# Optimization experiments

Hardware: AMD Instinct MI355X
Metric: run time of the kernel (lower is better)

Reference implementation:

```python
import jax, jax.numpy as jnp
import numpy as np

SIZE = 14          # feature-map side (448 image / stride 32)
IMG_STRIDE = 32    # feature->image coordinate stride
RATIOS = [(4, 4), (3, 5), (5, 3), (6, 6), (5, 7), (7, 5), (8, 8), (6, 10), (10, 6)]
GROUPS = [(0, 3), (3, 6), (6, 9)]   # ratio index ranges per scale group
N_LIST = [3, 2, 1]                   # proposals kept per group (sum = proposalN = 6)
IOU_THRESHS = [0.25, 0.25, 0.25]
WIN_NUMS = [(SIZE - h + 1) * (SIZE - w + 1) for h, w in RATIOS]  # 121,120,120,81,80,80,49,45,45
OFFS = np.cumsum([0] + WIN_NUMS)


def _make_coords():
    # image-space [x0,y0,x1,y1] per window, same order as flattened avgpool outputs
    coords = []
    for h, w in RATIOS:
        Ho, Wo = SIZE - h + 1, SIZE - w + 1
        for i in range(Ho):
            for j in range(Wo):
                x0 = i * IMG_STRIDE - 1
                y0 = j * IMG_STRIDE - 1
                x1 = x0 + h * IMG_STRIDE
                y1 = y0 + w * IMG_STRIDE
                coords.append([max(x0, 0), max(y0, 0), x1, y1])
    return np.asarray(coords, np.int32)  # [741, 4]


def setup_inputs() -> dict:
    key = jax.random.key(0)
    B = 65536
    x = jax.random.normal(key, (B, 1, SIZE, SIZE), dtype=jnp.float32)
    coords = jnp.asarray(_make_coords())
    return {"x": x, "coords": coords, "proposalN": 6}


def _avgpool_scores(x):
    # x: [B,1,H,W] -> concat of flattened VALID avgpools, [B, sum(WIN_NUMS)]
    B = x.shape[0]
    outs = []
    for h, w in RATIOS:
        s = jax.lax.reduce_window(x, 0.0, jax.lax.add, (1, 1, h, w), (1, 1, 1, 1), 'VALID')
        outs.append((s / (h * w)).reshape(B, -1))
    return jnp.concatenate(outs, axis=1)


def _nms_group(scores, coords_f, areas, N, thresh):
    # greedy NMS: repeatedly take argmax of remaining scores, suppress IoU>thresh.
    # Matches the torch/numpy loop (sorted-walk == repeated argmax for distinct scores).
    W = scores.shape[0]
    def step(carry, _):
        mask, last = carry
        any_v = jnp.any(mask)
        idx = jnp.argmax(jnp.where(mask, scores, -jnp.inf)).astype(jnp.int32)
        idx = jnp.where(any_v, idx, last)  # if exhausted, repeat last pick (as original)
        c = coords_f[idx]
        lx = jnp.minimum(coords_f[:, 2], c[2]) - jnp.maximum(coords_f[:, 0], c[0]) + 1.0
        ly = jnp.minimum(coords_f[:, 3], c[3]) - jnp.maximum(coords_f[:, 1], c[1]) + 1.0
        inter = jnp.where((lx < 0) | (ly < 0), 0.0, lx * ly)
        iou = inter / (areas + areas[idx] - inter)
        return (mask & (iou <= thresh), idx), idx
    init = (jnp.ones((W,), dtype=bool), jnp.int32(0))
    _, idxs = jax.lax.scan(step, init, None, length=N)
    return idxs  # [N] int32


def reference(x, coords, proposalN):
    all_scores = _avgpool_scores(x)                 # [B, 741]
    coords_f = coords.astype(jnp.float32)
    areas = (coords_f[:, 2] - coords_f[:, 0] + 1.0) * (coords_f[:, 3] - coords_f[:, 1] + 1.0)
    idx_parts = []
    for g, (a, b) in enumerate(GROUPS):
        s, e = int(OFFS[a]), int(OFFS[b])
        cf, ar = coords_f[s:e], areas[s:e]
        N, t = N_LIST[g], IOU_THRESHS[g]
        f = lambda sc, cf=cf, ar=ar, N=N, t=t: _nms_group(sc, cf, ar, N, t)
        idx_parts.append(jax.vmap(f)(all_scores[:, s:e]) + s)  # [B, N]
    proposalN_indices = jnp.concatenate(idx_parts, axis=1)      # [B, proposalN]
    proposalN_windows_scores = jnp.take_along_axis(all_scores, proposalN_indices, axis=1)
    window_scores = all_scores
    return proposalN_indices, proposalN_windows_scores, window_scores
```

## Files before the change

kernel.cpp:

```cpp
#include <hip/hip_runtime.h>
#include <stdint.h>

#define NW 741
#define NEG_INF_KEY 0x007FFFFFu

typedef float f2 __attribute__((ext_vector_type(2)));

__device__ __forceinline__ unsigned score_key(float f) {
  const unsigned u = __float_as_uint(f);
  return (u & 0x80000000u) ? ~u : (u | 0x80000000u);
}
__device__ __forceinline__ float key_score(unsigned k) {
  return __uint_as_float((k & 0x80000000u) ? (k ^ 0x80000000u) : ~k);
}

template<int CTRL>
__device__ __forceinline__ void argmax_step(unsigned& k, int& i) {
  const unsigned tk = (unsigned)__builtin_amdgcn_update_dpp(0, (int)k, CTRL, 0xF, 0xF, true);
  const int ti = __builtin_amdgcn_update_dpp(0, i, CTRL, 0xF, 0xF, true);
  if (tk > k || (tk == k && ti < i)) { k = tk; i = ti; }
}
__device__ __forceinline__ void wave_argmax(unsigned& k, int& i) {
  argmax_step<0x111>(k, i);
  argmax_step<0x112>(k, i);
  argmax_step<0x114>(k, i);
  argmax_step<0x118>(k, i);
  argmax_step<0x142>(k, i);
  argmax_step<0x143>(k, i);
  k = (unsigned)__builtin_amdgcn_readlane((int)k, 63);
  i = __builtin_amdgcn_readlane(i, 63);
}

template<int H, int W, int OFF, int NS, int SB>
__device__ __forceinline__ void score_ratio2(const f2* __restrict__ im2,
                                             unsigned* __restrict__ kA,
                                             unsigned* __restrict__ kB,
                                             float* __restrict__ wrowA,
                                             float* __restrict__ wrowB,
                                             const int lane, const bool hasB) {
  constexpr int Wo = 14 - W + 1;
  constexpr int Ho = 14 - H + 1;
  constexpr int NWIN = Ho * Wo;
  constexpr int P = Wo + 2;
#pragma unroll
  for (int s = 0; s < NS; ++s) {
    const int o = lane + 64 * s;
    unsigned ka = 0u, kb = 0u;
    if (o < NWIN) {
      const int i = o / Wo, j = o - i * Wo;
      const int cp = (o / P) & 3;
      const f2* p = im2 + cp * 196 + (i * 14 + j);
      f2 acc = {0.0f, 0.0f};
#pragma unroll
      for (int di = 0; di < H; ++di)
#pragma unroll
        for (int dj = 0; dj < W; ++dj)
          acc += p[di * 14 + dj];
      const float scA = acc.x / (float)(H * W);
      const float scB = acc.y / (float)(H * W);
      wrowA[OFF + o] = scA;
      if (hasB) wrowB[OFF + o] = scB;
      ka = score_key(scA);
      kb = score_key(scB);
    }
    kA[SB + s] = ka;
    kB[SB + s] = kb;
  }
}

__global__ __launch_bounds__(256, 4) void appm_kernel(
    const float* __restrict__ x, const int* __restrict__ coords,
    float* __restrict__ out, int B) {

  __shared__ float4 c_box[NW];
  __shared__ float c_ar[NW];
  __shared__ f2 imgp[4][784];

  const int t = threadIdx.x;
  const int wv = t >> 6;
  const int lane = t & 63;
  const int img0 = blockIdx.x * 8;
  const int imgA = img0 + wv * 2;
  const int imgB = imgA + 1;
  const bool hasA = (imgA < B);
  const bool hasB = (imgB < B);

  for (int w = t; w < NW; w += 256) {
    const int4 c = ((const int4*)coords)[w];
    const float fx0 = (float)c.x, fy0 = (float)c.y;
    const float fx1 = (float)c.z, fy1 = (float)c.w;
    c_box[w] = make_float4(fx0, fy0, fx1, fy1);
    c_ar[w] = (fx1 - fx0 + 1.0f) * (fy1 - fy0 + 1.0f);
  }

  {
    int nimg = B - img0; if (nimg > 8) nimg = 8;
    const int lim = nimg * 196;
    const float* xb = x + (long long)img0 * 196;
    for (int u = t; u < lim; u += 256) {
      const int i = u / 196, k = u - i * 196;
      const float v = xb[u];
      float* dst = (float*)imgp[i >> 1];
      const int fi = k * 2 + (i & 1);
#pragma unroll
      for (int cp = 0; cp < 4; ++cp)
        dst[cp * 392 + fi] = v;
    }
  }
  __syncthreads();

  if (hasA) {
    const f2* im2 = imgp[wv];
    float* wrowA = out + (long long)B * 12 + (long long)imgA * NW;
    float* wrowB = wrowA + NW;

    unsigned kA[15], kB[15];

    score_ratio2<4, 4, 0, 2, 0>(im2, kA, kB, wrowA, wrowB, lane, hasB);
    score_ratio2<3, 5, 121, 2, 2>(im2, kA, kB, wrowA, wrowB, lane, hasB);
    score_ratio2<5, 3, 241, 2, 4>(im2, kA, kB, wrowA, wrowB, lane, hasB);
    score_ratio2<6, 6, 361, 2, 6>(im2, kA, kB, wrowA, wrowB, lane, hasB);
    score_ratio2<5, 7, 442, 2, 8>(im2, kA, kB, wrowA, wrowB, lane, hasB);
    score_ratio2<7, 5, 522, 2, 10>(im2, kA, kB, wrowA, wrowB, lane, hasB);
    score_ratio2<8, 8, 602, 1, 12>(im2, kA, kB, wrowA, wrowB, lane, hasB);
    score_ratio2<6, 10, 651, 1, 13>(im2, kA, kB, wrowA, wrowB, lane, hasB);
    score_ratio2<10, 6, 696, 1, 14>(im2, kA, kB, wrowA, wrowB, lane, hasB);

    constexpr int SBASE[15] = {0, 64, 121, 185, 241, 305, 361, 425,
                               442, 506, 522, 586, 602, 651, 696};
    constexpr int GS[3] = {0, 6, 12};
    constexpr int GE[3] = {6, 12, 15};
    constexpr int GN[3] = {3, 2, 1};
    constexpr int GW0[3] = {0, 361, 602};

    float myIA = 0.0f, mySA = 0.0f, myIB = 0.0f, mySB = 0.0f;
    int pick = 0;
#pragma unroll
    for (int g = 0; g < 3; ++g) {
      int lastA = GW0[g], lastB = GW0[g];
      float lastSA = 0.0f, lastSB = 0.0f;
#pragma unroll
      for (int n = 0; n < GN[g]; ++n) {
        unsigned bkA = 0u, bkB = 0u;
        int biA = 0, biB = 0;
#pragma unroll
        for (int s = GS[g]; s < GE[g]; ++s) {
          const int o = SBASE[s] + lane;
          if (kA[s] > bkA) { bkA = kA[s]; biA = o; }
          if (kB[s] > bkB) { bkB = kB[s]; biB = o; }
        }
        wave_argmax(bkA, biA);
        wave_argmax(bkB, biB);

        int idxA, idxB; float scA, scB;
        if (bkA > NEG_INF_KEY) { idxA = biA; scA = key_score(bkA); }
        else { idxA = lastA; scA = lastSA; }
        if (bkB > NEG_INF_KEY) { idxB = biB; scB = key_score(bkB); }
        else { idxB = lastB; scB = lastSB; }
        lastA = idxA; lastSA = scA;
        lastB = idxB; lastSB = scB;
        if (lane == pick) { myIA = (float)idxA; mySA = scA; myIB = (float)idxB; mySB = scB; }
        pick++;

        if (n + 1 < GN[g]) {
          const float4 bA = c_box[idxA]; const float aA = c_ar[idxA];
          const float4 bB = c_box[idxB]; const float aB = c_ar[idxB];
#pragma unroll
          for (int s = GS[g]; s < GE[g]; ++s) {
            const int o = SBASE[s] + lane;
            const int oc = (o < NW) ? o : (NW - 1);
            const float4 cb = c_box[oc];
            const float ar = c_ar[oc];
            const float lxA = fminf(cb.z, bA.z) - fmaxf(cb.x, bA.x) + 1.0f;
            const float lyA = fminf(cb.w, bA.w) - fmaxf(cb.y, bA.y) + 1.0f;
            const float inA = (lxA < 0.0f || lyA < 0.0f) ? 0.0f : lxA * lyA;
            const bool supA = (4.0f * inA > ar + aA - inA);
            const float lxB = fminf(cb.z, bB.z) - fmaxf(cb.x, bB.x) + 1.0f;
            const float lyB = fminf(cb.w, bB.w) - fmaxf(cb.y, bB.y) + 1.0f;
            const float inB = (lxB < 0.0f || lyB < 0.0f) ? 0.0f : lxB * lyB;
            const bool supB = (4.0f * inB > ar + aB - inB);
            if (supA) kA[s] = 0u;
            if (supB) kB[s] = 0u;
          }
        }
      }
    }

    if (lane < 6) {
      const long long a6 = (long long)imgA * 6 + lane;
      out[a6] = myIA;
      out[(long long)B * 6 + a6] = mySA;
      if (hasB) {
        const long long b6 = (long long)imgB * 6 + lane;
        out[b6] = myIB;
        out[(long long)B * 6 + b6] = mySB;
      }
    }
  }
}

extern "C" void kernel_launch(void* const* d_in, const int* in_sizes, int n_in,
                              void* d_out, int out_size, void* d_ws, size_t ws_size,
                              hipStream_t stream) {
  const float* x = (const float*)d_in[0];
  const int* coords = (const int*)d_in[1];
  float* out = (float*)d_out;
  const int B = in_sizes[0] / 196;
  const int nblk = (B + 7) / 8;
  appm_kernel<<<dim3(nblk), dim3(256), 0, stream>>>(x, coords, out, B);
}
```

Measured before the change: 399.5 us.

## Shrink shared memory, drop image replicas, split wave argmax into max+min passes

The four-way replicated image copy in LDS, used to spread bank accesses, is replaced by a single interleaved pair copy, and the per-window area table is dropped and recomputed from the box. Together these cut LDS per block substantially, and launch bounds are raised to target 8 blocks per CU. The wave argmax now does a key-only DPP max, then a masked min-index reduction, instead of shuffling key and index together. In exchange it accepts possible LDS bank conflicts on image reads and a few extra FLOPs per IoU test.

```diff
diff --git a/kernel.cpp b/kernel.cpp
--- a/kernel.cpp
+++ b/kernel.cpp
@@ -15,20 +15,33 @@
 }
 
 template<int CTRL>
-__device__ __forceinline__ void argmax_step(unsigned& k, int& i) {
-  const unsigned tk = (unsigned)__builtin_amdgcn_update_dpp(0, (int)k, CTRL, 0xF, 0xF, true);
-  const int ti = __builtin_amdgcn_update_dpp(0, i, CTRL, 0xF, 0xF, true);
-  if (tk > k || (tk == k && ti < i)) { k = tk; i = ti; }
+__device__ __forceinline__ unsigned max_step(unsigned m) {
+  const unsigned t = (unsigned)__builtin_amdgcn_update_dpp(0, (int)m, CTRL, 0xF, 0xF, true);
+  return m > t ? m : t;
+}
+template<int CTRL>
+__device__ __forceinline__ int min_step(int c) {
+  const int t = __builtin_amdgcn_update_dpp(0x7fffffff, c, CTRL, 0xF, 0xF, false);
+  return c < t ? c : t;
 }
 __device__ __forceinline__ void wave_argmax(unsigned& k, int& i) {
-  argmax_step<0x111>(k, i);
-  argmax_step<0x112>(k, i);
-  argmax_step<0x114>(k, i);
-  argmax_step<0x118>(k, i);
-  argmax_step<0x142>(k, i);
-  argmax_step<0x143>(k, i);
-  k = (unsigned)__builtin_amdgcn_readlane((int)k, 63);
-  i = __builtin_amdgcn_readlane(i, 63);
+  unsigned m = k;
+  m = max_step<0x111>(m);
+  m = max_step<0x112>(m);
+  m = max_step<0x114>(m);
+  m = max_step<0x118>(m);
+  m = max_step<0x142>(m);
+  m = max_step<0x143>(m);
+  const unsigned smax = (unsigned)__builtin_amdgcn_readlane((int)m, 63);
+  int ci = (k == smax) ? i : 0x7fffffff;
+  ci = min_step<0x111>(ci);
+  ci = min_step<0x112>(ci);
+  ci = min_step<0x114>(ci);
+  ci = min_step<0x118>(ci);
+  ci = min_step<0x142>(ci);
+  ci = min_step<0x143>(ci);
+  k = smax;
+  i = __builtin_amdgcn_readlane(ci, 63);
 }
 
 template<int H, int W, int OFF, int NS, int SB>
@@ -41,15 +54,13 @@
   constexpr int Wo = 14 - W + 1;
   constexpr int Ho = 14 - H + 1;
   constexpr int NWIN = Ho * Wo;
-  constexpr int P = Wo + 2;
 #pragma unroll
   for (int s = 0; s < NS; ++s) {
     const int o = lane + 64 * s;
     unsigned ka = 0u, kb = 0u;
     if (o < NWIN) {
       const int i = o / Wo, j = o - i * Wo;
-      const int cp = (o / P) & 3;
-      const f2* p = im2 + cp * 196 + (i * 14 + j);
+      const f2* p = im2 + (i * 14 + j);
       f2 acc = {0.0f, 0.0f};
 #pragma unroll
       for (int di = 0; di < H; ++di)
@@ -68,13 +79,12 @@
   }
 }
 
-__global__ __launch_bounds__(256, 4) void appm_kernel(
+__global__ __launch_bounds__(256, 8) void appm_kernel(
     const float* __restrict__ x, const int* __restrict__ coords,
     float* __restrict__ out, int B) {
 
   __shared__ float4 c_box[NW];
-  __shared__ float c_ar[NW];
-  __shared__ f2 imgp[4][784];
+  __shared__ f2 imgp[4][196];
 
   const int t = threadIdx.x;
   const int wv = t >> 6;
@@ -87,24 +97,19 @@
 
   for (int w = t; w < NW; w += 256) {
     const int4 c = ((const int4*)coords)[w];
-    const float fx0 = (float)c.x, fy0 = (float)c.y;
-    const float fx1 = (float)c.z, fy1 = (float)c.w;
-    c_box[w] = make_float4(fx0, fy0, fx1, fy1);
-    c_ar[w] = (fx1 - fx0 + 1.0f) * (fy1 - fy0 + 1.0f);
+    c_box[w] = make_float4((float)c.x, (float)c.y, (float)c.z, (float)c.w);
   }
 
   {
     int nimg = B - img0; if (nimg > 8) nimg = 8;
-    const int lim = nimg * 196;
     const float* xb = x + (long long)img0 * 196;
-    for (int u = t; u < lim; u += 256) {
-      const int i = u / 196, k = u - i * 196;
-      const float v = xb[u];
-      float* dst = (float*)imgp[i >> 1];
-      const int fi = k * 2 + (i & 1);
-#pragma unroll
-      for (int cp = 0; cp < 4; ++cp)
-        dst[cp * 392 + fi] = v;
+    for (int u = t; u < 784; u += 256) {
+      const int pr = u / 196, k = u - pr * 196;
+      const int iA = 2 * pr, iB = iA + 1;
+      f2 v;
+      v.x = (iA < nimg) ? xb[iA * 196 + k] : 0.0f;
+      v.y = (iB < nimg) ? xb[iB * 196 + k] : 0.0f;
+      imgp[pr][k] = v;
     }
   }
   __syncthreads();
@@ -163,14 +168,16 @@
         pick++;
 
         if (n + 1 < GN[g]) {
-          const float4 bA = c_box[idxA]; const float aA = c_ar[idxA];
-          const float4 bB = c_box[idxB]; const float aB = c_ar[idxB];
+          const float4 bA = c_box[idxA];
+          const float4 bB = c_box[idxB];
+          const float aA = (bA.z - bA.x + 1.0f) * (bA.w - bA.y + 1.0f);
+          const float aB = (bB.z - bB.x + 1.0f) * (bB.w - bB.y + 1.0f);
 #pragma unroll
           for (int s = GS[g]; s < GE[g]; ++s) {
             const int o = SBASE[s] + lane;
             const int oc = (o < NW) ? o : (NW - 1);
             const float4 cb = c_box[oc];
-            const float ar = c_ar[oc];
+            const float ar = (cb.z - cb.x + 1.0f) * (cb.w - cb.y + 1.0f);
             const float lxA = fminf(cb.z, bA.z) - fmaxf(cb.x, bA.x) + 1.0f;
             const float lyA = fminf(cb.w, bA.w) - fmaxf(cb.y, bA.y) + 1.0f;
             const float inA = (lxA < 0.0f || lyA < 0.0f) ? 0.0f : lxA * lyA;
```

Result: faster. 380.2 us (-4.8%).
